# Performance work log

Measured on AMD Instinct MI355X. Metric: run time of the kernel, lower is better.

## Reference

```python
import jax, jax.numpy as jnp
import numpy as np

B, S, ENC, DEC, ATTN = 64, 2048, 512, 512, 256

def setup_inputs() -> dict:
    key = jax.random.key(0)
    k1, k2, k3, k4, k5 = jax.random.split(key, 5)
    s = 0.05
    return {
        "enc_outputs": jax.random.normal(k1, (B, S, ENC), dtype=jnp.float32),
        "dec_state": jax.random.normal(k2, (B, DEC), dtype=jnp.float32),
        "W_enc": jax.random.normal(k3, (ENC, ATTN), dtype=jnp.float32) * s,
        "W_dec": jax.random.normal(k4, (DEC, ATTN), dtype=jnp.float32) * s,
        "v": jax.random.normal(k5, (ATTN,), dtype=jnp.float32) * s,
    }

def reference(enc_outputs, dec_state, W_enc, W_dec, v):
    # enc_proj: [B,S,A], dec_proj: [B,1,A]
    enc_proj = jnp.einsum('bse,ea->bsa', enc_outputs, W_enc)
    dec_proj = jnp.einsum('bd,da->ba', dec_state, W_dec)[:, None, :]
    scores = jnp.einsum('bsa,a->bs', jnp.tanh(enc_proj + dec_proj), v)  # [B,S]
    attn_weights = jax.nn.softmax(scores, axis=-1)
    context = jnp.einsum('bs,bse->be', attn_weights, enc_outputs)  # [B,ENC]
    return (context, attn_weights)
```

## Files before the change

### kernel.cpp

```cpp
#include <hip/hip_runtime.h>
#include <hip/hip_bf16.h>
#include <stdint.h>

#define B_    64
#define S_    2048
#define ENC_  512
#define ATTN_ 256

typedef __bf16 bf16;
typedef bf16  bf16x8 __attribute__((ext_vector_type(8)));
typedef float f32x4  __attribute__((ext_vector_type(4)));

__device__ __forceinline__ float fexp2(float x) {
#if __has_builtin(__builtin_amdgcn_exp2f)
    return __builtin_amdgcn_exp2f(x);
#else
    return exp2f(x);
#endif
}
__device__ __forceinline__ float frcp(float x) {
#if __has_builtin(__builtin_amdgcn_rcpf)
    return __builtin_amdgcn_rcpf(x);
#else
    return 1.0f / x;
#endif
}
__device__ __forceinline__ float fast_tanh(float x) {
    float e = fexp2(x * 2.8853900817779268f);
    return 1.0f - 2.0f * frcp(e + 1.0f);
}

__device__ __forceinline__ void async_copy16(const void* g, void* l) {
#if __has_builtin(__builtin_amdgcn_global_load_lds)
    __builtin_amdgcn_global_load_lds(
        (__attribute__((address_space(1))) void*)(g),
        (__attribute__((address_space(3))) void*)(l), 16, 0, 0);
#else
    *(uint4*)l = *(const uint4*)g;
#endif
}

__global__ __launch_bounds__(256) void k_setup(const float* __restrict__ W_enc,
                                               const float* __restrict__ dec_state,
                                               const float* __restrict__ W_dec,
                                               bf16* __restrict__ WT,
                                               float* __restrict__ dp) {
    int blk = blockIdx.x;
    if (blk < 512) {
        int idx = blk * 256 + threadIdx.x;
        int n = idx >> 9;
        int k = idx & 511;
        WT[idx] = (bf16)W_enc[k * ATTN_ + n];
    } else {
        int b = blk - 512;
        int a = threadIdx.x;
        const float* ds = dec_state + b * 512;
        float acc = 0.f;
#pragma unroll 8
        for (int d = 0; d < 512; ++d)
            acc += ds[d] * W_dec[d * ATTN_ + a];
        dp[b * ATTN_ + a] = acc;
    }
}

__global__ __launch_bounds__(256, 2) void k_scores(
    const float* __restrict__ enc,
    const bf16*  __restrict__ WT,
    const float* __restrict__ dp,
    const float* __restrict__ v,
    float* __restrict__ out_scores)
{
    __shared__ __align__(16) bf16 As[128 * 40];
    __shared__ __align__(16) bf16 Bs[256 * 32];
    __shared__ float partial[4][64];

    const int tid  = threadIdx.x;
    const int wave = tid >> 6;
    const int lane = tid & 63;
    const int l15  = lane & 15;
    const int q    = lane >> 4;
    const int m0   = blockIdx.x * 128;
    const int b    = blockIdx.x >> 4;

    const int mrow0 = (wave >> 1) * 64;
    const int ncol0 = (wave & 1) * 128;

    float dpv[8], vv[8];
#pragma unroll
    for (int nt = 0; nt < 8; ++nt) {
        int col = ncol0 + nt * 16 + l15;
        dpv[nt] = dp[b * 256 + col];
        vv[nt]  = v[col];
    }

    const f32x4 zero4 = {0.f, 0.f, 0.f, 0.f};
    f32x4 acc[4][8];
#pragma unroll
    for (int mt = 0; mt < 4; ++mt)
#pragma unroll
        for (int nt = 0; nt < 8; ++nt)
            acc[mt][nt] = zero4;

    const int arow = tid >> 1;
    const int akc  = tid & 1;
    const float* ag = enc + (size_t)(m0 + arow) * 512 + akc * 16;
    bf16* as_dst = &As[arow * 40 + akc * 16];

    const int bcol4 = tid >> 2;
    const int bslot = tid & 3;

    for (int ks = 0; ks < 16; ++ks) {
#pragma unroll
        for (int r = 0; r < 4; ++r) {
            int c = r * 64 + bcol4;
            int g = bslot ^ ((c + (c >> 2)) & 3);
            async_copy16(WT + (size_t)c * 512 + ks * 32 + g * 8,
                         &Bs[r * 2048 + tid * 8]);
        }
        {
            const float* s = ag + ks * 32;
            float4 f0 = *(const float4*)(s);
            float4 f1 = *(const float4*)(s + 4);
            float4 f2 = *(const float4*)(s + 8);
            float4 f3 = *(const float4*)(s + 12);
            bf16x8 lo, hi;
            lo[0]=(bf16)f0.x; lo[1]=(bf16)f0.y; lo[2]=(bf16)f0.z; lo[3]=(bf16)f0.w;
            lo[4]=(bf16)f1.x; lo[5]=(bf16)f1.y; lo[6]=(bf16)f1.z; lo[7]=(bf16)f1.w;
            hi[0]=(bf16)f2.x; hi[1]=(bf16)f2.y; hi[2]=(bf16)f2.z; hi[3]=(bf16)f2.w;
            hi[4]=(bf16)f3.x; hi[5]=(bf16)f3.y; hi[6]=(bf16)f3.z; hi[7]=(bf16)f3.w;
            *(bf16x8*)(as_dst)     = lo;
            *(bf16x8*)(as_dst + 8) = hi;
        }
        __syncthreads();

        bf16x8 af[4];
#pragma unroll
        for (int mt = 0; mt < 4; ++mt) {
            int row = mrow0 + mt * 16 + l15;
            af[mt] = *(const bf16x8*)(&As[row * 40 + q * 8]);
        }
        bf16x8 bfr[8];
#pragma unroll
        for (int nt = 0; nt < 8; ++nt) {
            int col = ncol0 + nt * 16 + l15;
            int p = q ^ ((col + (col >> 2)) & 3);
            bfr[nt] = *(const bf16x8*)(&Bs[col * 32 + p * 8]);
        }
#pragma unroll
        for (int mt = 0; mt < 4; ++mt)
#pragma unroll
            for (int nt = 0; nt < 8; ++nt)
                acc[mt][nt] = __builtin_amdgcn_mfma_f32_16x16x32_bf16(af[mt], bfr[nt], acc[mt][nt], 0, 0, 0);
        __syncthreads();
    }

#pragma unroll
    for (int mt = 0; mt < 4; ++mt) {
#pragma unroll
        for (int r = 0; r < 4; ++r) {
            float s = 0.f;
#pragma unroll
            for (int nt = 0; nt < 8; ++nt)
                s += fast_tanh(acc[mt][nt][r] + dpv[nt]) * vv[nt];
            s += __shfl_xor(s, 1, 16);
            s += __shfl_xor(s, 2, 16);
            s += __shfl_xor(s, 4, 16);
            s += __shfl_xor(s, 8, 16);
            if (l15 == 0)
                partial[wave][mt * 16 + q * 4 + r] = s;
        }
    }
    __syncthreads();
    if (tid < 128) {
        int mw   = tid >> 6;
        int rloc = tid & 63;
        out_scores[m0 + mw * 64 + rloc] =
            partial[mw * 2][rloc] + partial[mw * 2 + 1][rloc];
    }
}

__global__ __launch_bounds__(256) void k_softmax(float* __restrict__ attn) {
    int b = blockIdx.x;
    float* s = attn + b * 2048;
    __shared__ float red[256];
    int tid = threadIdx.x;

    float x[8];
    float mx = -1e30f;
#pragma unroll
    for (int i = 0; i < 8; ++i) { x[i] = s[tid + 256 * i]; mx = fmaxf(mx, x[i]); }
    red[tid] = mx;
    __syncthreads();
    for (int off = 128; off > 0; off >>= 1) {
        if (tid < off) red[tid] = fmaxf(red[tid], red[tid + off]);
        __syncthreads();
    }
    mx = red[0];
    __syncthreads();

    float e[8];
    float lsum = 0.f;
#pragma unroll
    for (int i = 0; i < 8; ++i) { e[i] = fexp2((x[i] - mx) * 1.4426950408889634f); lsum += e[i]; }
    red[tid] = lsum;
    __syncthreads();
    for (int off = 128; off > 0; off >>= 1) {
        if (tid < off) red[tid] += red[tid + off];
        __syncthreads();
    }
    float inv = 1.0f / red[0];
#pragma unroll
    for (int i = 0; i < 8; ++i) s[tid + 256 * i] = e[i] * inv;
}

__global__ __launch_bounds__(256) void k_context(const float* __restrict__ enc,
                                                 const float* __restrict__ attn,
                                                 float* __restrict__ partial) {
    int b    = blockIdx.x >> 3;
    int slab = blockIdx.x & 7;
    int tid  = threadIdx.x;
    int eq   = tid & 127;
    int sr   = tid >> 7;
    const float* eb = enc + ((size_t)b * 2048 + slab * 256) * 512;
    const float* w  = attn + b * 2048 + slab * 256;

    f32x4 acc = {0.f, 0.f, 0.f, 0.f};
#pragma unroll 4
    for (int s = sr; s < 256; s += 2) {
        float ws = w[s];
        f32x4 ev = *(const f32x4*)(eb + (size_t)s * 512 + eq * 4);
        acc += ev * ws;
    }
    __shared__ f32x4 red[128];
    if (sr) red[eq] = acc;
    __syncthreads();
    if (!sr) {
        acc += red[eq];
        *(f32x4*)(partial + (size_t)blockIdx.x * 512 + eq * 4) = acc;
    }
}

__global__ __launch_bounds__(128) void k_ctxred(const float* __restrict__ partial,
                                                float* __restrict__ ctx) {
    int b  = blockIdx.x;
    int eq = threadIdx.x;
    f32x4 a = {0.f, 0.f, 0.f, 0.f};
#pragma unroll
    for (int slab = 0; slab < 8; ++slab)
        a += *(const f32x4*)(partial + ((size_t)b * 8 + slab) * 512 + eq * 4);
    *(f32x4*)(ctx + b * 512 + eq * 4) = a;
}

extern "C" void kernel_launch(void* const* d_in, const int* in_sizes, int n_in,
                              void* d_out, int out_size, void* d_ws, size_t ws_size,
                              hipStream_t stream) {
    const float* enc       = (const float*)d_in[0];
    const float* dec_state = (const float*)d_in[1];
    const float* W_enc     = (const float*)d_in[2];
    const float* W_dec     = (const float*)d_in[3];
    const float* v         = (const float*)d_in[4];

    float* ctx  = (float*)d_out;
    float* attn = (float*)d_out + 64 * 512;

    char*  ws      = (char*)d_ws;
    bf16*  WT      = (bf16*)ws;
    float* dp      = (float*)(ws + 256 * 1024);
    float* partial = (float*)(ws + 256 * 1024 + 64 * 1024);

    k_setup  <<<576, 256, 0, stream>>>(W_enc, dec_state, W_dec, WT, dp);
    k_scores <<<1024, 256, 0, stream>>>(enc, WT, dp, v, attn);
    k_softmax<<<64, 256, 0, stream>>>(attn);
    k_context<<<512, 256, 0, stream>>>(enc, attn, partial);
    k_ctxred <<<64, 128, 0, stream>>>(partial, ctx);
}
```

Baseline: 449.9 us.

## Double-buffer score GEMM tiles and fuse softmax into context kernel

The scores GEMM now double-buffers LDS tiles. It prefetches the fp32 encoder rows for two steps ahead into registers and issues the async weight copy for the next step before computing the current one, so there is one barrier per k-step instead of two. The standalone softmax kernel is removed. Each context block recomputes the row max and sum over its batch's 2048 scores, computes its own weights, and the slab-0 block writes the normalized attention. The context work is split into 16 slabs per batch, which adds redundant softmax reductions per block and doubles LDS and register use in the GEMM.

```diff
diff --git a/kernel.cpp b/kernel.cpp
--- a/kernel.cpp
+++ b/kernel.cpp
@@ -9,6 +9,7 @@
 
 typedef __bf16 bf16;
 typedef bf16  bf16x8 __attribute__((ext_vector_type(8)));
+typedef bf16  bf16x4 __attribute__((ext_vector_type(4)));
 typedef float f32x4  __attribute__((ext_vector_type(4)));
 
 __device__ __forceinline__ float fexp2(float x) {
@@ -70,8 +71,8 @@
     const float* __restrict__ v,
     float* __restrict__ out_scores)
 {
-    __shared__ __align__(16) bf16 As[128 * 40];
-    __shared__ __align__(16) bf16 Bs[256 * 32];
+    __shared__ __align__(16) bf16 As[2][128 * 40];
+    __shared__ __align__(16) bf16 Bs[2][256 * 32];
     __shared__ float partial[4][64];
 
     const int tid  = threadIdx.x;
@@ -101,50 +102,63 @@
         for (int nt = 0; nt < 8; ++nt)
             acc[mt][nt] = zero4;
 
-    const int arow = tid >> 1;
-    const int akc  = tid & 1;
-    const float* ag = enc + (size_t)(m0 + arow) * 512 + akc * 16;
-    bf16* as_dst = &As[arow * 40 + akc * 16];
+    const int arow8 = tid >> 3;
+    const int acol8 = tid & 7;
+    const float* ag = enc + (size_t)(m0 + arow8) * 512 + acol8 * 4;
 
     const int bcol4 = tid >> 2;
     const int bslot = tid & 3;
 
-    for (int ks = 0; ks < 16; ++ks) {
+    float4 rcur[4], rnext[4];
+    auto loadA = [&](int ks, float4* r) {
+#pragma unroll
+        for (int rg = 0; rg < 4; ++rg)
+            r[rg] = *(const float4*)(ag + (size_t)rg * 32 * 512 + ks * 32);
+    };
+    auto writeA = [&](int p, const float4* r) {
+#pragma unroll
+        for (int rg = 0; rg < 4; ++rg) {
+            bf16x4 c;
+            c[0] = (bf16)r[rg].x; c[1] = (bf16)r[rg].y;
+            c[2] = (bf16)r[rg].z; c[3] = (bf16)r[rg].w;
+            *(bf16x4*)(&As[p][(rg * 32 + arow8) * 40 + acol8 * 4]) = c;
+        }
+    };
+    auto issueB = [&](int ks, int p) {
 #pragma unroll
         for (int r = 0; r < 4; ++r) {
             int c = r * 64 + bcol4;
             int g = bslot ^ ((c + (c >> 2)) & 3);
             async_copy16(WT + (size_t)c * 512 + ks * 32 + g * 8,
-                         &Bs[r * 2048 + tid * 8]);
-        }
-        {
-            const float* s = ag + ks * 32;
-            float4 f0 = *(const float4*)(s);
-            float4 f1 = *(const float4*)(s + 4);
-            float4 f2 = *(const float4*)(s + 8);
-            float4 f3 = *(const float4*)(s + 12);
-            bf16x8 lo, hi;
-            lo[0]=(bf16)f0.x; lo[1]=(bf16)f0.y; lo[2]=(bf16)f0.z; lo[3]=(bf16)f0.w;
-            lo[4]=(bf16)f1.x; lo[5]=(bf16)f1.y; lo[6]=(bf16)f1.z; lo[7]=(bf16)f1.w;
-            hi[0]=(bf16)f2.x; hi[1]=(bf16)f2.y; hi[2]=(bf16)f2.z; hi[3]=(bf16)f2.w;
-            hi[4]=(bf16)f3.x; hi[5]=(bf16)f3.y; hi[6]=(bf16)f3.z; hi[7]=(bf16)f3.w;
-            *(bf16x8*)(as_dst)     = lo;
-            *(bf16x8*)(as_dst + 8) = hi;
-        }
-        __syncthreads();
-
+                         &Bs[p][r * 2048 + tid * 8]);
+        }
+    };
+
+    loadA(0, rcur);
+    issueB(0, 0);
+    writeA(0, rcur);
+    loadA(1, rcur);
+    __syncthreads();
+
+    for (int ks = 0; ks < 16; ++ks) {
+        const int p = ks & 1;
+        if (ks < 14) loadA(ks + 2, rnext);
+        if (ks < 15) {
+            writeA(1 - p, rcur);
+            issueB(ks + 1, 1 - p);
+        }
         bf16x8 af[4];
 #pragma unroll
         for (int mt = 0; mt < 4; ++mt) {
             int row = mrow0 + mt * 16 + l15;
-            af[mt] = *(const bf16x8*)(&As[row * 40 + q * 8]);
+            af[mt] = *(const bf16x8*)(&As[p][row * 40 + q * 8]);
         }
         bf16x8 bfr[8];
 #pragma unroll
         for (int nt = 0; nt < 8; ++nt) {
             int col = ncol0 + nt * 16 + l15;
-            int p = q ^ ((col + (col >> 2)) & 3);
-            bfr[nt] = *(const bf16x8*)(&Bs[col * 32 + p * 8]);
+            int pc = q ^ ((col + (col >> 2)) & 3);
+            bfr[nt] = *(const bf16x8*)(&Bs[p][col * 32 + pc * 8]);
         }
 #pragma unroll
         for (int mt = 0; mt < 4; ++mt)
@@ -152,6 +166,8 @@
             for (int nt = 0; nt < 8; ++nt)
                 acc[mt][nt] = __builtin_amdgcn_mfma_f32_16x16x32_bf16(af[mt], bfr[nt], acc[mt][nt], 0, 0, 0);
         __syncthreads();
+#pragma unroll
+        for (int i = 0; i < 4; ++i) rcur[i] = rnext[i];
     }
 
 #pragma unroll
@@ -179,16 +195,23 @@
     }
 }
 
-__global__ __launch_bounds__(256) void k_softmax(float* __restrict__ attn) {
-    int b = blockIdx.x;
-    float* s = attn + b * 2048;
+__global__ __launch_bounds__(256) void k_context(const float* __restrict__ enc,
+                                                 const float* __restrict__ scores,
+                                                 float* __restrict__ attn_out,
+                                                 float* __restrict__ partial) {
+    const int b    = blockIdx.x >> 4;
+    const int slab = blockIdx.x & 15;
+    const int tid  = threadIdx.x;
+    const float* sc = scores + b * 2048;
+
     __shared__ float red[256];
-    int tid = threadIdx.x;
+    __shared__ float wl[128];
+    __shared__ f32x4 r2[128];
 
     float x[8];
     float mx = -1e30f;
 #pragma unroll
-    for (int i = 0; i < 8; ++i) { x[i] = s[tid + 256 * i]; mx = fmaxf(mx, x[i]); }
+    for (int i = 0; i < 8; ++i) { x[i] = sc[tid + 256 * i]; mx = fmaxf(mx, x[i]); }
     red[tid] = mx;
     __syncthreads();
     for (int off = 128; off > 0; off >>= 1) {
@@ -197,46 +220,44 @@
     }
     mx = red[0];
     __syncthreads();
-
-    float e[8];
-    float lsum = 0.f;
-#pragma unroll
-    for (int i = 0; i < 8; ++i) { e[i] = fexp2((x[i] - mx) * 1.4426950408889634f); lsum += e[i]; }
-    red[tid] = lsum;
+    float e[8], ls = 0.f;
+#pragma unroll
+    for (int i = 0; i < 8; ++i) { e[i] = fexp2((x[i] - mx) * 1.4426950408889634f); ls += e[i]; }
+    red[tid] = ls;
     __syncthreads();
     for (int off = 128; off > 0; off >>= 1) {
         if (tid < off) red[tid] += red[tid + off];
         __syncthreads();
     }
-    float inv = 1.0f / red[0];
-#pragma unroll
-    for (int i = 0; i < 8; ++i) s[tid + 256 * i] = e[i] * inv;
-}
-
-__global__ __launch_bounds__(256) void k_context(const float* __restrict__ enc,
-                                                 const float* __restrict__ attn,
-                                                 float* __restrict__ partial) {
-    int b    = blockIdx.x >> 3;
-    int slab = blockIdx.x & 7;
-    int tid  = threadIdx.x;
-    int eq   = tid & 127;
-    int sr   = tid >> 7;
-    const float* eb = enc + ((size_t)b * 2048 + slab * 256) * 512;
-    const float* w  = attn + b * 2048 + slab * 256;
-
+    const float inv = 1.0f / red[0];
+
+    if (tid < 128) {
+        float s0 = sc[slab * 128 + tid];
+        wl[tid] = fexp2((s0 - mx) * 1.4426950408889634f) * inv;
+    }
+    if (slab == 0) {
+#pragma unroll
+        for (int i = 0; i < 8; ++i)
+            attn_out[b * 2048 + tid + 256 * i] = e[i] * inv;
+    }
+    __syncthreads();
+
+    const float* eb = enc + ((size_t)b * 2048 + slab * 128) * 512;
+    const int half = tid >> 7;
+    const int col4 = tid & 127;
     f32x4 acc = {0.f, 0.f, 0.f, 0.f};
-#pragma unroll 4
-    for (int s = sr; s < 256; s += 2) {
-        float ws = w[s];
-        f32x4 ev = *(const f32x4*)(eb + (size_t)s * 512 + eq * 4);
+#pragma unroll 8
+    for (int s2 = 0; s2 < 64; ++s2) {
+        int row = s2 * 2 + half;
+        float ws = wl[row];
+        f32x4 ev = *(const f32x4*)(eb + (size_t)row * 512 + col4 * 4);
         acc += ev * ws;
     }
-    __shared__ f32x4 red[128];
-    if (sr) red[eq] = acc;
-    __syncthreads();
-    if (!sr) {
-        acc += red[eq];
-        *(f32x4*)(partial + (size_t)blockIdx.x * 512 + eq * 4) = acc;
+    if (half) r2[col4] = acc;
+    __syncthreads();
+    if (!half) {
+        acc += r2[col4];
+        *(f32x4*)(partial + (size_t)blockIdx.x * 512 + col4 * 4) = acc;
     }
 }
 
@@ -246,8 +267,8 @@
     int eq = threadIdx.x;
     f32x4 a = {0.f, 0.f, 0.f, 0.f};
 #pragma unroll
-    for (int slab = 0; slab < 8; ++slab)
-        a += *(const f32x4*)(partial + ((size_t)b * 8 + slab) * 512 + eq * 4);
+    for (int slab = 0; slab < 16; ++slab)
+        a += *(const f32x4*)(partial + ((size_t)b * 16 + slab) * 512 + eq * 4);
     *(f32x4*)(ctx + b * 512 + eq * 4) = a;
 }
 
@@ -263,14 +284,14 @@
     float* ctx  = (float*)d_out;
     float* attn = (float*)d_out + 64 * 512;
 
-    char*  ws      = (char*)d_ws;
-    bf16*  WT      = (bf16*)ws;
-    float* dp      = (float*)(ws + 256 * 1024);
-    float* partial = (float*)(ws + 256 * 1024 + 64 * 1024);
+    char*  ws        = (char*)d_ws;
+    bf16*  WT        = (bf16*)ws;
+    float* dp        = (float*)(ws + 262144);
+    float* scores_ws = (float*)(ws + 262144 + 65536);
+    float* partial   = (float*)(ws + 262144 + 65536 + 524288);
 
     k_setup  <<<576, 256, 0, stream>>>(W_enc, dec_state, W_dec, WT, dp);
-    k_scores <<<1024, 256, 0, stream>>>(enc, WT, dp, v, attn);
-    k_softmax<<<64, 256, 0, stream>>>(attn);
-    k_context<<<512, 256, 0, stream>>>(enc, attn, partial);
+    k_scores <<<1024, 256, 0, stream>>>(enc, WT, dp, v, scores_ws);
+    k_context<<<1024, 256, 0, stream>>>(enc, scores_ws, attn, partial);
     k_ctxred <<<64, 128, 0, stream>>>(partial, ctx);
 }
```

After: 452.3 us. Within noise of the previous version (+0.5%).
